# Optimization experiments

Measured on AMD Instinct MI355X. Metric: run time of the kernel, lower is better.

The kernel has to match this reference:

```python
import jax, jax.numpy as jnp
import numpy as np

D_MODEL = 1024
NHEADS = 16
D_K = D_MODEL // NHEADS


def setup_inputs() -> dict:
    key = jax.random.key(0)
    ks = jax.random.split(key, 12)
    B, S = 2, 2048
    scale = 1.0 / np.sqrt(D_MODEL)
    inp = {
        "query": jax.random.normal(ks[0], (B, S, D_MODEL), dtype=jnp.float32),
        "key": jax.random.normal(ks[1], (B, S, D_MODEL), dtype=jnp.float32),
        "value": jax.random.normal(ks[2], (B, S, D_MODEL), dtype=jnp.float32),
        "mask": jax.random.randint(ks[3], (B, 1, S, S), 0, 2, dtype=jnp.int32),
        "Wq": jax.random.normal(ks[4], (D_MODEL, D_MODEL), dtype=jnp.float32) * scale,
        "bq": jnp.zeros((D_MODEL,), dtype=jnp.float32),
        "Wk": jax.random.normal(ks[5], (D_MODEL, D_MODEL), dtype=jnp.float32) * scale,
        "bk": jnp.zeros((D_MODEL,), dtype=jnp.float32),
        "Wv": jax.random.normal(ks[6], (D_MODEL, D_MODEL), dtype=jnp.float32) * scale,
        "bv": jnp.zeros((D_MODEL,), dtype=jnp.float32),
        "Wo": jax.random.normal(ks[7], (D_MODEL, D_MODEL), dtype=jnp.float32) * scale,
        "bo": jnp.zeros((D_MODEL,), dtype=jnp.float32),
    }
    return inp


def _split_heads(x):
    # [B, S, (H*D)] -> [B, H, S, D]
    B, S, _ = x.shape
    return x.reshape(B, S, NHEADS, D_K).transpose(0, 2, 1, 3)


def reference(query, key, value, mask, Wq, bq, Wk, bk, Wv, bv, Wo, bo):
    B, Sq, _ = query.shape
    q = _split_heads(query @ Wq + bq)            # [B, H, Sq, Dk]
    k = _split_heads(key @ Wk + bk)              # [B, H, Sk, Dk]
    v = _split_heads(value @ Wv + bv)            # [B, H, Sk, Dk]
    # scores: [B, H, Sq, Sk], scaled by sqrt(d_k)
    scores = jnp.einsum("bhqd,bhkd->bhqk", q, k) / np.sqrt(D_K).astype(np.float32)
    scores = jnp.where(mask == 0, jnp.float32(-1e12), scores)
    weights = jax.nn.softmax(scores, axis=-1)
    out = jnp.einsum("bhqk,bhkd->bhqd", weights, v)  # [B, H, Sq, Dk]
    out = out.transpose(0, 2, 1, 3).reshape(B, Sq, D_MODEL)
    return out @ Wo + bo  # dropout is identity in eval / p=0
```

## Files before the change

kernel.cpp:

```cpp
#include <hip/hip_runtime.h>
#include <math.h>

#define D_MODEL 1024
#define NHEADS  16
#define DK      64
#define BATCH   2
#define SEQ     2048
#define M_TOTAL (BATCH * SEQ)
#define NT      (SEQ / 64)
#define CK1 0.18033688011112042f
#define CK0 -17.312340490667561f

typedef __attribute__((ext_vector_type(8))) short bf16x8;
typedef __attribute__((ext_vector_type(4))) float f32x4;

__device__ __forceinline__ unsigned short f2bf(float f) {
    union { float f; unsigned int i; } v; v.f = f;
    return (unsigned short)((v.i + 0x7FFFu + ((v.i >> 16) & 1u)) >> 16);
}

__device__ __forceinline__ void async_copy16(const void* g, void* l) {
    __builtin_amdgcn_global_load_lds(
        (const __attribute__((address_space(1))) unsigned int*)g,
        (__attribute__((address_space(3))) unsigned int*)l, 16, 0, 0);
}

struct Cvt3 { const float* s[3]; unsigned short* d[3]; };
__global__ __launch_bounds__(256)
void cvt_flat(const Cvt3 a)
{
    const float* __restrict__ s = a.s[blockIdx.z];
    unsigned short* __restrict__ d = a.d[blockIdx.z];
    const size_t i = ((size_t)blockIdx.x * 256 + threadIdx.x) * 4;
    const float4 v = *reinterpret_cast<const float4*>(&s[i]);
    ushort4 o;
    o.x = f2bf(v.x); o.y = f2bf(v.y); o.z = f2bf(v.z); o.w = f2bf(v.w);
    *reinterpret_cast<ushort4*>(&d[i]) = o;
}

struct Cvt4 { const float* s[4]; unsigned short* d[4]; };
__global__ __launch_bounds__(256)
void cvt_wt(const Cvt4 a)
{
    __shared__ unsigned short t[32][33];
    const float* __restrict__ W = a.s[blockIdx.z];
    unsigned short* __restrict__ WT = a.d[blockIdx.z];
    const int tx = threadIdx.x & 31;
    const int ty = threadIdx.x >> 5;
    const int nb = blockIdx.x << 5;
    const int kb = blockIdx.y << 5;
#pragma unroll
    for (int i = 0; i < 4; ++i)
        t[ty + (i << 3)][tx] = f2bf(W[(size_t)(kb + ty + (i << 3)) * D_MODEL + nb + tx]);
    __syncthreads();
#pragma unroll
    for (int i = 0; i < 4; ++i)
        WT[(size_t)(nb + ty + (i << 3)) * D_MODEL + kb + tx] = t[tx][ty + (i << 3)];
}

__global__ __launch_bounds__(256)
void mask_pack(const int* __restrict__ mask, unsigned long long* __restrict__ wm)
{
    const int tid  = threadIdx.x;
    const int lane = tid & 63;
    const int l15  = lane & 15;
    const int kg   = lane >> 4;
    const int wv   = ((int)blockIdx.x << 2) + (tid >> 6);
    const int t    = wv & 31;
    const int qw   = (wv >> 5) & 127;
    const int bb   = wv >> 12;

    const int* mb = mask + (size_t)bb * SEQ * SEQ
                  + (size_t)((qw << 4) + l15) * SEQ + (t << 6) + (kg << 2);
    unsigned long long* wout = wm + ((((size_t)bb * 128 + qw) * 32 + t) << 4);

    int4 ln[4];
#pragma unroll
    for (int n = 0; n < 4; ++n)
        ln[n] = *reinterpret_cast<const int4*>(mb + (n << 4));
#pragma unroll
    for (int r = 0; r < 4; ++r)
#pragma unroll
        for (int n = 0; n < 4; ++n) {
            const int mvv = (&ln[n].x)[r];
            const unsigned long long bal = __ballot(mvv != 0);
            if (lane == 0) wout[(r << 2) | n] = bal;
        }
}

template <typename OutT> struct GArgs {
    const unsigned short* X[3];
    const unsigned short* W[3];
    const float*          Bi[3];
    OutT*                 O[3];
};

__device__ __forceinline__ void st_out(float* p, float v) { *p = v; }
__device__ __forceinline__ void st_out(unsigned short* p, float v) { *p = f2bf(v); }

template <typename OutT>
__global__ __launch_bounds__(256)
void gemm_bf16(const GArgs<OutT> args, const int head_split)
{
    __shared__ __align__(16) unsigned short As[128][32];
    __shared__ __align__(16) unsigned short Bs[128][32];

    const unsigned short* __restrict__ X  = args.X[blockIdx.z];
    const unsigned short* __restrict__ WT = args.W[blockIdx.z];
    const float* __restrict__ bias        = args.Bi[blockIdx.z];
    OutT* __restrict__ out                = args.O[blockIdx.z];

    const int tid = threadIdx.x;
    const int wid = tid >> 6;
    const int wy  = wid >> 1;
    const int wx  = wid & 1;
    const int l15 = tid & 15;
    const int kg  = (tid >> 4) & 3;

    const int id = ((int)blockIdx.y << 3) | (int)blockIdx.x;
    const int sw = ((id & 7) << 5) | (id >> 3);
    const int n0 = (sw & 7) << 7;
    const int m0 = (sw >> 3) << 7;

    const int lane = tid & 63;
    const int gr   = lane >> 2;
    const int gc   = (lane & 3) << 3;
    const int c0   = wid << 1;

    f32x4 acc[4][4];
#pragma unroll
    for (int i = 0; i < 4; ++i)
#pragma unroll
        for (int j = 0; j < 4; ++j)
            acc[i][j] = (f32x4){0.f, 0.f, 0.f, 0.f};

#pragma unroll 1
    for (int t = 0; t < D_MODEL / 32; ++t) {
        const int k0 = t << 5;

        __syncthreads();
#pragma unroll
        for (int cc = 0; cc < 2; ++cc) {
            const int c = c0 + cc;
            async_copy16(&X[(size_t)(m0 + (c << 4) + gr) * D_MODEL + k0 + gc],
                         &As[c << 4][0]);
            async_copy16(&WT[(size_t)(n0 + (c << 4) + gr) * D_MODEL + k0 + gc],
                         &Bs[c << 4][0]);
        }
        __syncthreads();

        bf16x8 a[4], b[4];
#pragma unroll
        for (int i = 0; i < 4; ++i)
            a[i] = *reinterpret_cast<const bf16x8*>(
                &As[(wy << 6) + (i << 4) + l15][kg << 3]);
#pragma unroll
        for (int j = 0; j < 4; ++j)
            b[j] = *reinterpret_cast<const bf16x8*>(
                &Bs[(wx << 6) + (j << 4) + l15][kg << 3]);
#pragma unroll
        for (int i = 0; i < 4; ++i)
#pragma unroll
            for (int j = 0; j < 4; ++j)
                acc[i][j] = __builtin_amdgcn_mfma_f32_16x16x32_bf16(
                    a[i], b[j], acc[i][j], 0, 0, 0);
    }

    float bv[4];
#pragma unroll
    for (int j = 0; j < 4; ++j)
        bv[j] = bias[n0 + (wx << 6) + (j << 4) + l15];

#pragma unroll
    for (int i = 0; i < 4; ++i) {
#pragma unroll
        for (int r = 0; r < 4; ++r) {
            const int m = m0 + (wy << 6) + (i << 4) + (kg << 2) + r;
#pragma unroll
            for (int j = 0; j < 4; ++j) {
                const int n = n0 + (wx << 6) + (j << 4) + l15;
                const float val = acc[i][j][r] + bv[j];
                if (head_split) {
                    const int bbx = m >> 11;
                    const int ss  = m & (SEQ - 1);
                    const int hhx = n >> 6;
                    const int dd  = n & (DK - 1);
                    st_out(&out[((size_t)(bbx * NHEADS + hhx) * SEQ + ss) * DK + dd], val);
                } else {
                    st_out(&out[(size_t)m * D_MODEL + n], val);
                }
            }
        }
    }
}

__global__ __launch_bounds__(256)
void flash_mfma(const unsigned short* __restrict__ Qb,
                const unsigned short* __restrict__ Kb,
                const unsigned short* __restrict__ Vb,
                const unsigned long long* __restrict__ wmask,
                unsigned short* __restrict__ ctx)
{
    __shared__ __align__(16) unsigned short Kbf[2][64][72];
    __shared__ __align__(16) unsigned short V3 [2][64][72];

    const int tid  = threadIdx.x;
    const int w    = tid >> 6;
    const int lane = tid & 63;
    const int l15  = lane & 15;
    const int kg   = lane >> 4;

    const int flat = ((int)blockIdx.z * NHEADS + (int)blockIdx.y) * (SEQ / 128)
                   + (int)blockIdx.x;
    const int swz  = ((flat & 7) << 6) | (flat >> 3);
    const int q0 = (swz & 15) << 7;
    const int hh = (swz >> 4) & 15;
    const int bb = swz >> 8;

    const unsigned short* Qh = Qb + (size_t)(bb * NHEADS + hh) * SEQ * DK;
    const unsigned short* Kh = Kb + (size_t)(bb * NHEADS + hh) * SEQ * DK;
    const unsigned short* Vh = Vb + (size_t)(bb * NHEADS + hh) * SEQ * DK;

    bf16x8 aq[2][2];
#pragma unroll
    for (int qi = 0; qi < 2; ++qi) {
        const unsigned short* qrow =
            Qh + (size_t)(q0 + w * 32 + qi * 16 + l15) * DK + (kg << 3);
        aq[qi][0] = *reinterpret_cast<const bf16x8*>(qrow);
        aq[qi][1] = *reinterpret_cast<const bf16x8*>(qrow + 32);
    }

    const int krow = tid >> 2;
    const int kcb  = (tid & 3) << 4;
    const int vkb  = (tid & 15) << 2;
    const int vdb  = (tid >> 4) << 2;
    const int voff = (((vkb >> 2) & 3) << 4) + ((vkb >> 4) << 2);

    const int wbase0 = __builtin_amdgcn_readfirstlane(
        (bb * 128 + (q0 >> 4) + (w << 1)) << 9);
    const int wbase1 = wbase0 + 512;

    float lsum[2] = {0.f, 0.f};
    f32x4 O4[2][4];
#pragma unroll
    for (int qi = 0; qi < 2; ++qi)
#pragma unroll
        for (int db = 0; db < 4; ++db) O4[qi][db] = (f32x4){0.f, 0.f, 0.f, 0.f};

    uint4 kv0 = *reinterpret_cast<const uint4*>(Kh + (size_t)krow * DK + kcb);
    uint4 kv1 = *reinterpret_cast<const uint4*>(Kh + (size_t)krow * DK + kcb + 8);
    uint2 vr[4];
#pragma unroll
    for (int i = 0; i < 4; ++i)
        vr[i] = *reinterpret_cast<const uint2*>(Vh + (size_t)(vkb + i) * DK + vdb);

#pragma unroll 1
    for (int t = 0; t < NT; ++t) {
        const int c = t & 1;

        *reinterpret_cast<uint4*>(&Kbf[c][krow][kcb])     = kv0;
        *reinterpret_cast<uint4*>(&Kbf[c][krow][kcb + 8]) = kv1;
        {
            uint2 o;
            o.x = (vr[0].x & 0xFFFFu) | (vr[1].x << 16);
            o.y = (vr[2].x & 0xFFFFu) | (vr[3].x << 16);
            *reinterpret_cast<uint2*>(&V3[c][vdb + 0][voff]) = o;
            o.x = (vr[0].x >> 16) | (vr[1].x & 0xFFFF0000u);
            o.y = (vr[2].x >> 16) | (vr[3].x & 0xFFFF0000u);
            *reinterpret_cast<uint2*>(&V3[c][vdb + 1][voff]) = o;
            o.x = (vr[0].y & 0xFFFFu) | (vr[1].y << 16);
            o.y = (vr[2].y & 0xFFFFu) | (vr[3].y << 16);
            *reinterpret_cast<uint2*>(&V3[c][vdb + 2][voff]) = o;
            o.x = (vr[0].y >> 16) | (vr[1].y & 0xFFFF0000u);
            o.y = (vr[2].y >> 16) | (vr[3].y & 0xFFFF0000u);
            *reinterpret_cast<uint2*>(&V3[c][vdb + 3][voff]) = o;
        }
        __syncthreads();

        if (t + 1 < NT) {
            const int kn = (t + 1) << 6;
            kv0 = *reinterpret_cast<const uint4*>(Kh + (size_t)(kn + krow) * DK + kcb);
            kv1 = *reinterpret_cast<const uint4*>(Kh + (size_t)(kn + krow) * DK + kcb + 8);
#pragma unroll
            for (int i = 0; i < 4; ++i)
                vr[i] = *reinterpret_cast<const uint2*>(
                    Vh + (size_t)(kn + vkb + i) * DK + vdb);
        }

        f32x4 S[2][4];
#pragma unroll
        for (int n = 0; n < 4; ++n) {
            const bf16x8 b0 = *reinterpret_cast<const bf16x8*>(
                &Kbf[c][16 * n + l15][kg << 3]);
            const bf16x8 b1 = *reinterpret_cast<const bf16x8*>(
                &Kbf[c][16 * n + l15][(kg << 3) + 32]);
#pragma unroll
            for (int qi = 0; qi < 2; ++qi) {
                f32x4 acc = (f32x4){0.f, 0.f, 0.f, 0.f};
                acc = __builtin_amdgcn_mfma_f32_16x16x32_bf16(b0, aq[qi][0], acc, 0, 0, 0);
                acc = __builtin_amdgcn_mfma_f32_16x16x32_bf16(b1, aq[qi][1], acc, 0, 0, 0);
                S[qi][n] = acc;
            }
        }

        bf16x8 paf[2][2];
#pragma unroll
        for (int qi = 0; qi < 2; ++qi) {
            const unsigned long long* wmt =
                wmask + (qi ? wbase1 : wbase0) + (t << 4);
            unsigned long long wmv[16];
#pragma unroll
            for (int rn = 0; rn < 16; ++rn) wmv[rn] = wmt[rn];

            unsigned pw01[4], pw23[4];
#pragma unroll
            for (int n = 0; n < 4; ++n) {
                float xv[4];
#pragma unroll
                for (int r = 0; r < 4; ++r) {
                    float e = fmaf(S[qi][n][r], CK1, CK0);
                    __asm__("v_exp_f32 %0, %1" : "=v"(e) : "v"(e));
                    __asm__("v_cndmask_b32 %0, 0, %1, %2"
                            : "=v"(e) : "v"(e), "s"(wmv[(r << 2) | n]));
                    xv[r] = e;
                }
                lsum[qi] += (xv[0] + xv[1]) + (xv[2] + xv[3]);
                __asm__("v_cvt_pk_bf16_f32 %0, %1, %2"
                        : "=v"(pw01[n]) : "v"(xv[0]), "v"(xv[1]));
                __asm__("v_cvt_pk_bf16_f32 %0, %1, %2"
                        : "=v"(pw23[n]) : "v"(xv[2]), "v"(xv[3]));
            }
            union { unsigned u[4]; bf16x8 v; } pa0, pa1;
            pa0.u[0] = pw01[0]; pa0.u[1] = pw23[0]; pa0.u[2] = pw01[1]; pa0.u[3] = pw23[1];
            pa1.u[0] = pw01[2]; pa1.u[1] = pw23[2]; pa1.u[2] = pw01[3]; pa1.u[3] = pw23[3];
            paf[qi][0] = pa0.v;
            paf[qi][1] = pa1.v;
        }

#pragma unroll
        for (int db = 0; db < 4; ++db) {
            const unsigned short* vbase = &V3[c][(db << 4) + l15][kg << 4];
            const bf16x8 v0 = *reinterpret_cast<const bf16x8*>(vbase);
            const bf16x8 v1 = *reinterpret_cast<const bf16x8*>(vbase + 8);
#pragma unroll
            for (int qi = 0; qi < 2; ++qi) {
                O4[qi][db] = __builtin_amdgcn_mfma_f32_16x16x32_bf16(
                    paf[qi][0], v0, O4[qi][db], 0, 0, 0);
                O4[qi][db] = __builtin_amdgcn_mfma_f32_16x16x32_bf16(
                    paf[qi][1], v1, O4[qi][db], 0, 0, 0);
            }
        }
    }

#pragma unroll
    for (int qi = 0; qi < 2; ++qi) {
        float ls = lsum[qi];
        ls += __shfl_xor(ls, 16);
        ls += __shfl_xor(ls, 32);
#pragma unroll
        for (int r = 0; r < 4; ++r) {
            const float rs = __shfl(ls, (kg << 2) + r);
            const float inv = 1.f / rs;
            const size_t base =
                (size_t)(bb * SEQ + q0 + w * 32 + qi * 16 + (kg << 2) + r) * D_MODEL
                + hh * DK + l15;
#pragma unroll
            for (int db = 0; db < 4; ++db)
                ctx[base + 16 * db] = f2bf(O4[qi][db][r] * inv);
        }
    }
}

extern "C" void kernel_launch(void* const* d_in, const int* in_sizes, int n_in,
                              void* d_out, int out_size, void* d_ws, size_t ws_size,
                              hipStream_t stream)
{
    const float* query = (const float*)d_in[0];
    const float* key   = (const float*)d_in[1];
    const float* value = (const float*)d_in[2];
    const int*   mask  = (const int*)d_in[3];
    const float* Wq = (const float*)d_in[4];
    const float* bq = (const float*)d_in[5];
    const float* Wk = (const float*)d_in[6];
    const float* bk = (const float*)d_in[7];
    const float* Wv = (const float*)d_in[8];
    const float* bv = (const float*)d_in[9];
    const float* Wo = (const float*)d_in[10];
    const float* bo = (const float*)d_in[11];

    unsigned short* ws = (unsigned short*)d_ws;
    const size_t TE = (size_t)M_TOTAL * D_MODEL;
    const size_t WE = (size_t)D_MODEL * D_MODEL;
    unsigned short* Xq  = ws;
    unsigned short* Xk  = Xq + TE;
    unsigned short* Xv  = Xk + TE;
    unsigned short* WTq = Xv + TE;
    unsigned short* WTk = WTq + WE;
    unsigned short* WTv = WTk + WE;
    unsigned short* WTo = WTv + WE;
    unsigned short* Qb  = WTo + WE;
    unsigned short* Kb  = Qb + TE;
    unsigned short* Vb  = Kb + TE;
    unsigned short* Ctx = Vb + TE;
    unsigned long long* WM = (unsigned long long*)(Ctx + TE);

    Cvt3 c3;
    c3.s[0] = query; c3.s[1] = key; c3.s[2] = value;
    c3.d[0] = Xq;    c3.d[1] = Xk;  c3.d[2] = Xv;
    cvt_flat<<<dim3(TE / 1024, 1, 3), 256, 0, stream>>>(c3);

    Cvt4 c4;
    c4.s[0] = Wq;  c4.s[1] = Wk;  c4.s[2] = Wv;  c4.s[3] = Wo;
    c4.d[0] = WTq; c4.d[1] = WTk; c4.d[2] = WTv; c4.d[3] = WTo;
    cvt_wt<<<dim3(32, 32, 4), 256, 0, stream>>>(c4);

    mask_pack<<<dim3(2048, 1, 1), 256, 0, stream>>>(mask, WM);

    GArgs<unsigned short> qkv;
    qkv.X[0] = Xq;  qkv.X[1] = Xk;  qkv.X[2] = Xv;
    qkv.W[0] = WTq; qkv.W[1] = WTk; qkv.W[2] = WTv;
    qkv.Bi[0] = bq; qkv.Bi[1] = bk; qkv.Bi[2] = bv;
    qkv.O[0] = Qb;  qkv.O[1] = Kb;  qkv.O[2] = Vb;
    gemm_bf16<unsigned short><<<dim3(8, 32, 3), 256, 0, stream>>>(qkv, 1);

    flash_mfma<<<dim3(SEQ / 128, NHEADS, BATCH), 256, 0, stream>>>(
        Qb, Kb, Vb, WM, Ctx);

    GArgs<float> op;
    op.X[0] = Ctx;  op.X[1] = Ctx;  op.X[2] = Ctx;
    op.W[0] = WTo;  op.W[1] = WTo;  op.W[2] = WTo;
    op.Bi[0] = bo;  op.Bi[1] = bo;  op.Bi[2] = bo;
    op.O[0] = (float*)d_out; op.O[1] = (float*)d_out; op.O[2] = (float*)d_out;
    gemm_bf16<float><<<dim3(8, 32, 1), 256, 0, stream>>>(op, 0);
}
```

Baseline: 272.3 us.

## Merge prep kernels into one launch, add MFMA priority hints, regrid output GEMM

The three preprocessing kernels (activation bf16 conversion, weight transpose-convert, mask bit-packing) are merged into a single kernel that dispatches on block index, removing two launches and their inter-kernel gaps. The flash attention loop wraps its two MFMA phases in s_setprio so matrix work is favoured over the exp/mask phase across waves. The output-projection GEMM is relaunched as an (8,16,2) grid that splits M tiles over z, with the tile swizzle generalised to the grid's y size. The merged kernel loses per-phase grid shaping, and every branch reserves the transpose shared buffer.

```diff
diff --git a/kernel.cpp b/kernel.cpp
--- a/kernel.cpp
+++ b/kernel.cpp
@@ -25,67 +25,77 @@
         (__attribute__((address_space(3))) unsigned int*)l, 16, 0, 0);
 }
 
-struct Cvt3 { const float* s[3]; unsigned short* d[3]; };
+struct PrepArgs {
+    const float* xs[3]; unsigned short* xd[3];
+    const float* wsrc[4]; unsigned short* wdst[4];
+    const int* mask; unsigned long long* wm;
+};
+
 __global__ __launch_bounds__(256)
-void cvt_flat(const Cvt3 a)
+void prep_all(const PrepArgs a)
 {
-    const float* __restrict__ s = a.s[blockIdx.z];
-    unsigned short* __restrict__ d = a.d[blockIdx.z];
-    const size_t i = ((size_t)blockIdx.x * 256 + threadIdx.x) * 4;
-    const float4 v = *reinterpret_cast<const float4*>(&s[i]);
-    ushort4 o;
-    o.x = f2bf(v.x); o.y = f2bf(v.y); o.z = f2bf(v.z); o.w = f2bf(v.w);
-    *reinterpret_cast<ushort4*>(&d[i]) = o;
-}
-
-struct Cvt4 { const float* s[4]; unsigned short* d[4]; };
-__global__ __launch_bounds__(256)
-void cvt_wt(const Cvt4 a)
-{
-    __shared__ unsigned short t[32][33];
-    const float* __restrict__ W = a.s[blockIdx.z];
-    unsigned short* __restrict__ WT = a.d[blockIdx.z];
-    const int tx = threadIdx.x & 31;
-    const int ty = threadIdx.x >> 5;
-    const int nb = blockIdx.x << 5;
-    const int kb = blockIdx.y << 5;
-#pragma unroll
-    for (int i = 0; i < 4; ++i)
-        t[ty + (i << 3)][tx] = f2bf(W[(size_t)(kb + ty + (i << 3)) * D_MODEL + nb + tx]);
-    __syncthreads();
-#pragma unroll
-    for (int i = 0; i < 4; ++i)
-        WT[(size_t)(nb + ty + (i << 3)) * D_MODEL + kb + tx] = t[tx][ty + (i << 3)];
-}
-
-__global__ __launch_bounds__(256)
-void mask_pack(const int* __restrict__ mask, unsigned long long* __restrict__ wm)
-{
-    const int tid  = threadIdx.x;
-    const int lane = tid & 63;
-    const int l15  = lane & 15;
-    const int kg   = lane >> 4;
-    const int wv   = ((int)blockIdx.x << 2) + (tid >> 6);
-    const int t    = wv & 31;
-    const int qw   = (wv >> 5) & 127;
-    const int bb   = wv >> 12;
-
-    const int* mb = mask + (size_t)bb * SEQ * SEQ
-                  + (size_t)((qw << 4) + l15) * SEQ + (t << 6) + (kg << 2);
-    unsigned long long* wout = wm + ((((size_t)bb * 128 + qw) * 32 + t) << 4);
-
-    int4 ln[4];
-#pragma unroll
-    for (int n = 0; n < 4; ++n)
-        ln[n] = *reinterpret_cast<const int4*>(mb + (n << 4));
-#pragma unroll
-    for (int r = 0; r < 4; ++r)
-#pragma unroll
-        for (int n = 0; n < 4; ++n) {
-            const int mvv = (&ln[n].x)[r];
-            const unsigned long long bal = __ballot(mvv != 0);
-            if (lane == 0) wout[(r << 2) | n] = bal;
-        }
+    __shared__ unsigned short tbuf[32][33];
+    const int id  = blockIdx.x;
+    const int tid = threadIdx.x;
+
+    if (id < 12288) {
+        const int z = id >> 12;
+        const int x = id & 4095;
+        const float* __restrict__ s = a.xs[z];
+        unsigned short* __restrict__ d = a.xd[z];
+        const size_t i = ((size_t)x * 256 + tid) * 4;
+        const float4 v = *reinterpret_cast<const float4*>(&s[i]);
+        ushort4 o;
+        o.x = f2bf(v.x); o.y = f2bf(v.y); o.z = f2bf(v.z); o.w = f2bf(v.w);
+        *reinterpret_cast<ushort4*>(&d[i]) = o;
+    } else if (id < 16384) {
+        const int r  = id - 12288;
+        const int z  = r >> 10;
+        const int rem = r & 1023;
+        const int bx = rem & 31;
+        const int by = rem >> 5;
+        const float* __restrict__ W = a.wsrc[z];
+        unsigned short* __restrict__ WT = a.wdst[z];
+        const int tx = tid & 31;
+        const int ty = tid >> 5;
+        const int nb = bx << 5;
+        const int kb = by << 5;
+#pragma unroll
+        for (int i = 0; i < 4; ++i)
+            tbuf[ty + (i << 3)][tx] =
+                f2bf(W[(size_t)(kb + ty + (i << 3)) * D_MODEL + nb + tx]);
+        __syncthreads();
+#pragma unroll
+        for (int i = 0; i < 4; ++i)
+            WT[(size_t)(nb + ty + (i << 3)) * D_MODEL + kb + tx] =
+                tbuf[tx][ty + (i << 3)];
+    } else {
+        const int bxm = id - 16384;
+        const int lane = tid & 63;
+        const int l15  = lane & 15;
+        const int kg   = lane >> 4;
+        const int wv   = (bxm << 2) + (tid >> 6);
+        const int t    = wv & 31;
+        const int qw   = (wv >> 5) & 127;
+        const int bb   = wv >> 12;
+
+        const int* mb = a.mask + (size_t)bb * SEQ * SEQ
+                      + (size_t)((qw << 4) + l15) * SEQ + (t << 6) + (kg << 2);
+        unsigned long long* wout = a.wm + ((((size_t)bb * 128 + qw) * 32 + t) << 4);
+
+        int4 ln[4];
+#pragma unroll
+        for (int n = 0; n < 4; ++n)
+            ln[n] = *reinterpret_cast<const int4*>(mb + (n << 4));
+#pragma unroll
+        for (int r = 0; r < 4; ++r)
+#pragma unroll
+            for (int n = 0; n < 4; ++n) {
+                const int mvv = (&ln[n].x)[r];
+                const unsigned long long bal = __ballot(mvv != 0);
+                if (lane == 0) wout[(r << 2) | n] = bal;
+            }
+    }
 }
 
 template <typename OutT> struct GArgs {
@@ -100,15 +110,16 @@
 
 template <typename OutT>
 __global__ __launch_bounds__(256)
-void gemm_bf16(const GArgs<OutT> args, const int head_split)
+void gemm_bf16(const GArgs<OutT> args, const int head_split, const int m_z_tiles)
 {
     __shared__ __align__(16) unsigned short As[128][32];
     __shared__ __align__(16) unsigned short Bs[128][32];
 
-    const unsigned short* __restrict__ X  = args.X[blockIdx.z];
-    const unsigned short* __restrict__ WT = args.W[blockIdx.z];
-    const float* __restrict__ bias        = args.Bi[blockIdx.z];
-    OutT* __restrict__ out                = args.O[blockIdx.z];
+    const int opz = m_z_tiles ? 0 : blockIdx.z;
+    const unsigned short* __restrict__ X  = args.X[opz];
+    const unsigned short* __restrict__ WT = args.W[opz];
+    const float* __restrict__ bias        = args.Bi[opz];
+    OutT* __restrict__ out                = args.O[opz];
 
     const int tid = threadIdx.x;
     const int wid = tid >> 6;
@@ -117,10 +128,11 @@
     const int l15 = tid & 15;
     const int kg  = (tid >> 4) & 3;
 
+    const int nwgy = (int)gridDim.y;
     const int id = ((int)blockIdx.y << 3) | (int)blockIdx.x;
-    const int sw = ((id & 7) << 5) | (id >> 3);
+    const int sw = (id & 7) * nwgy + (id >> 3);
     const int n0 = (sw & 7) << 7;
-    const int m0 = (sw >> 3) << 7;
+    const int m0 = ((sw >> 3) + (int)blockIdx.z * m_z_tiles) << 7;
 
     const int lane = tid & 63;
     const int gr   = lane >> 2;
@@ -288,6 +300,7 @@
         }
 
         f32x4 S[2][4];
+        __builtin_amdgcn_s_setprio(1);
 #pragma unroll
         for (int n = 0; n < 4; ++n) {
             const bf16x8 b0 = *reinterpret_cast<const bf16x8*>(
@@ -302,6 +315,7 @@
                 S[qi][n] = acc;
             }
         }
+        __builtin_amdgcn_s_setprio(0);
 
         bf16x8 paf[2][2];
 #pragma unroll
@@ -337,6 +351,7 @@
             paf[qi][1] = pa1.v;
         }
 
+        __builtin_amdgcn_s_setprio(1);
 #pragma unroll
         for (int db = 0; db < 4; ++db) {
             const unsigned short* vbase = &V3[c][(db << 4) + l15][kg << 4];
@@ -350,6 +365,7 @@
                     paf[qi][1], v1, O4[qi][db], 0, 0, 0);
             }
         }
+        __builtin_amdgcn_s_setprio(0);
     }
 
 #pragma unroll
@@ -404,24 +420,20 @@
     unsigned short* Ctx = Vb + TE;
     unsigned long long* WM = (unsigned long long*)(Ctx + TE);
 
-    Cvt3 c3;
-    c3.s[0] = query; c3.s[1] = key; c3.s[2] = value;
-    c3.d[0] = Xq;    c3.d[1] = Xk;  c3.d[2] = Xv;
-    cvt_flat<<<dim3(TE / 1024, 1, 3), 256, 0, stream>>>(c3);
-
-    Cvt4 c4;
-    c4.s[0] = Wq;  c4.s[1] = Wk;  c4.s[2] = Wv;  c4.s[3] = Wo;
-    c4.d[0] = WTq; c4.d[1] = WTk; c4.d[2] = WTv; c4.d[3] = WTo;
-    cvt_wt<<<dim3(32, 32, 4), 256, 0, stream>>>(c4);
-
-    mask_pack<<<dim3(2048, 1, 1), 256, 0, stream>>>(mask, WM);
+    PrepArgs pa;
+    pa.xs[0] = query; pa.xs[1] = key; pa.xs[2] = value;
+    pa.xd[0] = Xq;    pa.xd[1] = Xk;  pa.xd[2] = Xv;
+    pa.wsrc[0] = Wq;  pa.wsrc[1] = Wk;  pa.wsrc[2] = Wv;  pa.wsrc[3] = Wo;
+    pa.wdst[0] = WTq; pa.wdst[1] = WTk; pa.wdst[2] = WTv; pa.wdst[3] = WTo;
+    pa.mask = mask; pa.wm = WM;
+    prep_all<<<dim3(18432, 1, 1), 256, 0, stream>>>(pa);
 
     GArgs<unsigned short> qkv;
     qkv.X[0] = Xq;  qkv.X[1] = Xk;  qkv.X[2] = Xv;
     qkv.W[0] = WTq; qkv.W[1] = WTk; qkv.W[2] = WTv;
     qkv.Bi[0] = bq; qkv.Bi[1] = bk; qkv.Bi[2] = bv;
     qkv.O[0] = Qb;  qkv.O[1] = Kb;  qkv.O[2] = Vb;
-    gemm_bf16<unsigned short><<<dim3(8, 32, 3), 256, 0, stream>>>(qkv, 1);
+    gemm_bf16<unsigned short><<<dim3(8, 32, 3), 256, 0, stream>>>(qkv, 1, 0);
 
     flash_mfma<<<dim3(SEQ / 128, NHEADS, BATCH), 256, 0, stream>>>(
         Qb, Kb, Vb, WM, Ctx);
@@ -431,5 +443,5 @@
     op.W[0] = WTo;  op.W[1] = WTo;  op.W[2] = WTo;
     op.Bi[0] = bo;  op.Bi[1] = bo;  op.Bi[2] = bo;
     op.O[0] = (float*)d_out; op.O[1] = (float*)d_out; op.O[2] = (float*)d_out;
-    gemm_bf16<float><<<dim3(8, 32, 1), 256, 0, stream>>>(op, 0);
-}
+    gemm_bf16<float><<<dim3(8, 16, 2), 256, 0, stream>>>(op, 0, 16);
+}
```

After: 271.8 us. Within noise of the previous version (-0.2%).
